# Kernel tuning notes

Hardware: AMD Instinct MI355X
Metric: run time of the kernel (lower is better)

The kernel has to match this reference:

```python
import jax, jax.numpy as jnp
import numpy as np

D_MODEL = 1024
N_HEADS = 16
D_HEAD = D_MODEL // N_HEADS
D_FF = 4 * D_MODEL
SEQ = 2048
BATCH = 4
EPS = 1e-5


def setup_inputs() -> dict:
    key = jax.random.key(0)
    ks = jax.random.split(key, 12)
    s = 0.02
    return {
        "x": jax.random.normal(ks[0], (BATCH, SEQ, D_MODEL), dtype=jnp.float32),
        "ln1_g": jnp.ones((D_MODEL,), jnp.float32),
        "ln1_b": jnp.zeros((D_MODEL,), jnp.float32),
        "wq": jax.random.normal(ks[1], (N_HEADS, D_MODEL, D_HEAD), jnp.float32) * s,
        "bq": jnp.zeros((N_HEADS, D_HEAD), jnp.float32),
        "wk": jax.random.normal(ks[2], (N_HEADS, D_MODEL, D_HEAD), jnp.float32) * s,
        "bk": jnp.zeros((N_HEADS, D_HEAD), jnp.float32),
        "wv": jax.random.normal(ks[3], (N_HEADS, D_MODEL, D_HEAD), jnp.float32) * s,
        "bv": jnp.zeros((N_HEADS, D_HEAD), jnp.float32),
        "wp": jax.random.normal(ks[4], (D_MODEL, D_MODEL), jnp.float32) * s,
        "bp": jnp.zeros((D_MODEL,), jnp.float32),
        "ln2_g": jnp.ones((D_MODEL,), jnp.float32),
        "ln2_b": jnp.zeros((D_MODEL,), jnp.float32),
        "w1": jax.random.normal(ks[5], (D_MODEL, D_FF), jnp.float32) * s,
        "b1": jnp.zeros((D_FF,), jnp.float32),
        "w2": jax.random.normal(ks[6], (D_FF, D_MODEL), jnp.float32) * s,
        "b2": jnp.zeros((D_MODEL,), jnp.float32),
    }


def _layer_norm(x, g, b):
    mu = jnp.mean(x, axis=-1, keepdims=True)
    var = jnp.mean(jnp.square(x - mu), axis=-1, keepdims=True)
    return (x - mu) * jax.lax.rsqrt(var + EPS) * g + b


def _block(x, ln1_g, ln1_b, wq, bq, wk, bk, wv, bv, wp, bp,
           ln2_g, ln2_b, w1, b1, w2, b2):
    B, S, D = x.shape
    # --- pre-LN multi-head causal self-attention ---
    xn = _layer_norm(x, ln1_g, ln1_b)
    q = jnp.einsum('bsd,hde->bhse', xn, wq) + bq[None, :, None, :]
    k = jnp.einsum('bsd,hde->bhse', xn, wk) + bk[None, :, None, :]
    v = jnp.einsum('bsd,hde->bhse', xn, wv) + bv[None, :, None, :]
    scores = jnp.einsum('bhse,bhte->bhst', q, k) / np.sqrt(D_HEAD).astype(np.float32)
    causal = jnp.tril(jnp.ones((S, S), dtype=bool))
    scores = jnp.where(causal[None, None], scores, jnp.float32(-jnp.inf))
    attn = jax.nn.softmax(scores, axis=-1)
    o = jnp.einsum('bhst,bhte->bhse', attn, v)          # [B,H,S,Dh]
    o = o.transpose(0, 2, 1, 3).reshape(B, S, D)         # concat heads
    x = x + o @ wp + bp
    # --- pre-LN feedforward ---
    xn2 = _layer_norm(x, ln2_g, ln2_b)
    h = jax.nn.relu(xn2 @ w1 + b1)
    x = x + h @ w2 + b2
    return x


def reference(x, ln1_g, ln1_b, wq, bq, wk, bk, wv, bv, wp, bp,
              ln2_g, ln2_b, w1, b1, w2, b2):
    return _block(x, ln1_g, ln1_b, wq, bq, wk, bk, wv, bv, wp, bp,
                  ln2_g, ln2_b, w1, b1, w2, b2)
```

## Files before the change

### kernel.cpp

```cpp
#include <hip/hip_runtime.h>
#include <hip/hip_bf16.h>

#define D_MODEL 1024
#define N_HEADS 16
#define D_HEAD  64
#define D_FF    4096
#define SEQ     2048
#define BATCH   4
#define NROWS   (BATCH * SEQ)

typedef __attribute__((ext_vector_type(8))) short short8;
typedef __attribute__((ext_vector_type(4))) float f32x4;

#define EXP2(x) exp2f(x)
#define MFMA16(a, b, c) __builtin_amdgcn_mfma_f32_16x16x32_bf16(a, b, c, 0, 0, 0)

static __device__ __forceinline__ ushort f2bf(float x) {
  __hip_bfloat16 h = __float2bfloat16(x);
  return *reinterpret_cast<ushort*>(&h);
}
static __device__ __forceinline__ float bf2f(ushort u) {
  unsigned int v = ((unsigned int)u) << 16;
  return *reinterpret_cast<float*>(&v);
}

static __device__ __forceinline__ void gl_lds16(const ushort* g, ushort* l) {
  __builtin_amdgcn_global_load_lds(
      (const __attribute__((address_space(1))) void*)g,
      (__attribute__((address_space(3))) void*)l, 16, 0, 0);
}

struct PackArgs {
  const float* in[6];
  ushort* out[6];
  int K[6], N[6], nx[6], per_batch[6];
  long in_bs[6], out_bs[6];
  int cum[7];
};

__global__ __launch_bounds__(256) void pack_all(PackArgs a) {
  const int b = blockIdx.x;
  int j = 0;
#pragma unroll
  for (int i = 0; i < 5; ++i) if (b >= a.cum[i + 1]) j = i + 1;
  const int tidx = b - a.cum[j];
  const int bz = tidx / a.per_batch[j];
  const int rem = tidx % a.per_batch[j];
  const int n0 = (rem % a.nx[j]) * 32;
  const int k0 = (rem / a.nx[j]) * 32;
  const float* in = a.in[j] + (long)bz * a.in_bs[j];
  ushort* out = a.out[j] + (long)bz * a.out_bs[j];
  const int K = a.K[j], N = a.N[j];

  __shared__ float tile[32][33];
  const int tx = threadIdx.x, ty = threadIdx.y;
#pragma unroll
  for (int i = 0; i < 32; i += 8)
    tile[ty + i][tx] = in[(size_t)(k0 + ty + i) * N + n0 + tx];
  __syncthreads();
#pragma unroll
  for (int i = 0; i < 32; i += 8)
    out[(size_t)(n0 + ty + i) * K + k0 + tx] = f2bf(tile[tx][ty + i]);
}

__global__ __launch_bounds__(256) void ln_kernel(
    const float* __restrict__ x, const float* __restrict__ g,
    const float* __restrict__ b, ushort* __restrict__ out) {
  int row = blockIdx.x, t = threadIdx.x;
  const float4 v = *(const float4*)(x + (size_t)row * D_MODEL + t * 4);
  float s  = v.x + v.y + v.z + v.w;
  float ss = v.x * v.x + v.y * v.y + v.z * v.z + v.w * v.w;
#pragma unroll
  for (int off = 1; off < 64; off <<= 1) {
    s  += __shfl_xor(s, off, 64);
    ss += __shfl_xor(ss, off, 64);
  }
  __shared__ float rs_[4], rss_[4];
  int w = t >> 6;
  if ((t & 63) == 0) { rs_[w] = s; rss_[w] = ss; }
  __syncthreads();
  s  = rs_[0] + rs_[1] + rs_[2] + rs_[3];
  ss = rss_[0] + rss_[1] + rss_[2] + rss_[3];
  float mu  = s * (1.0f / D_MODEL);
  float var = ss * (1.0f / D_MODEL) - mu * mu;
  float rstd = rsqrtf(var + 1e-5f);
  float4 gg = *(const float4*)(g + t * 4);
  float4 bb = *(const float4*)(b + t * 4);
  ushort4 r;
  r.x = f2bf((v.x - mu) * rstd * gg.x + bb.x);
  r.y = f2bf((v.y - mu) * rstd * gg.y + bb.y);
  r.z = f2bf((v.z - mu) * rstd * gg.z + bb.z);
  r.w = f2bf((v.w - mu) * rstd * gg.w + bb.w);
  *(ushort4*)(out + (size_t)row * D_MODEL + t * 4) = r;
}

__global__ __launch_bounds__(256) void ln_bf16_kernel(
    const ushort* __restrict__ x, const float* __restrict__ g,
    const float* __restrict__ b, ushort* __restrict__ out) {
  int row = blockIdx.x, t = threadIdx.x;
  const ushort4 u = *(const ushort4*)(x + (size_t)row * D_MODEL + t * 4);
  float4 v;
  v.x = bf2f(u.x); v.y = bf2f(u.y); v.z = bf2f(u.z); v.w = bf2f(u.w);
  float s  = v.x + v.y + v.z + v.w;
  float ss = v.x * v.x + v.y * v.y + v.z * v.z + v.w * v.w;
#pragma unroll
  for (int off = 1; off < 64; off <<= 1) {
    s  += __shfl_xor(s, off, 64);
    ss += __shfl_xor(ss, off, 64);
  }
  __shared__ float rs_[4], rss_[4];
  int w = t >> 6;
  if ((t & 63) == 0) { rs_[w] = s; rss_[w] = ss; }
  __syncthreads();
  s  = rs_[0] + rs_[1] + rs_[2] + rs_[3];
  ss = rss_[0] + rss_[1] + rss_[2] + rss_[3];
  float mu  = s * (1.0f / D_MODEL);
  float var = ss * (1.0f / D_MODEL) - mu * mu;
  float rstd = rsqrtf(var + 1e-5f);
  float4 gg = *(const float4*)(g + t * 4);
  float4 bb = *(const float4*)(b + t * 4);
  ushort4 r;
  r.x = f2bf((v.x - mu) * rstd * gg.x + bb.x);
  r.y = f2bf((v.y - mu) * rstd * gg.y + bb.y);
  r.z = f2bf((v.z - mu) * rstd * gg.z + bb.z);
  r.w = f2bf((v.w - mu) * rstd * gg.w + bb.w);
  *(ushort4*)(out + (size_t)row * D_MODEL + t * 4) = r;
}

template <int MODE>
__global__ __launch_bounds__(512, 2) void gemm256(
    const ushort* __restrict__ A, const ushort* __restrict__ BT,
    int M, int N, int K,
    const float* __restrict__ bias0, const float* __restrict__ bias1,
    const float* __restrict__ bias2,
    void* __restrict__ out0, void* __restrict__ out1, void* __restrict__ out2) {
  __shared__ __align__(16) ushort As[2][256 * 64];
  __shared__ __align__(16) ushort Bs[2][256 * 64];
  const int gx = N >> 8;
  const int nwg = gx * (M >> 8);
  const int cpx = nwg >> 3;
  const int tile = (blockIdx.x & 7) * cpx + (blockIdx.x >> 3);
  const int bn = tile % gx, bm = tile / gx;
  const int t = threadIdx.x, lane = t & 63, w = t >> 6;
  const int wr = w >> 2, wc = w & 3;
  const int l16 = lane & 15, l4 = lane >> 4;

  const ushort* Ab = A + (size_t)(bm * 256) * K;
  const ushort* Bb = BT + (size_t)(bn * 256) * K;

  int srow[4], scol[4];
#pragma unroll
  for (int i = 0; i < 4; ++i) {
    int c = i * 512 + t;
    srow[i] = c >> 3;
    scol[i] = 8 * ((c & 7) ^ ((c >> 3) & 7));
  }

  f32x4 acc[8][4] = {};
  int cur = 0;
  const int nk = K >> 6;

#pragma unroll
  for (int i = 0; i < 4; ++i) {
    gl_lds16(&Ab[(size_t)srow[i] * K + scol[i]], (ushort*)&As[0][(i * 512 + w * 64) * 8]);
    gl_lds16(&Bb[(size_t)srow[i] * K + scol[i]], (ushort*)&Bs[0][(i * 512 + w * 64) * 8]);
  }

  for (int kt = 0; kt < nk; ++kt) {
    if (kt + 1 < nk) {
      const int k0n = (kt + 1) << 6;
#pragma unroll
      for (int i = 0; i < 4; ++i) {
        gl_lds16(&Ab[(size_t)srow[i] * K + k0n + scol[i]], (ushort*)&As[cur ^ 1][(i * 512 + w * 64) * 8]);
        gl_lds16(&Bb[(size_t)srow[i] * K + k0n + scol[i]], (ushort*)&Bs[cur ^ 1][(i * 512 + w * 64) * 8]);
      }
      asm volatile("s_waitcnt vmcnt(8)" ::: "memory");
    } else {
      asm volatile("s_waitcnt vmcnt(0)" ::: "memory");
    }
    __builtin_amdgcn_s_barrier();

    const ushort* As_ = As[cur];
    const ushort* Bs_ = Bs[cur];
    short8 bfr[4][2];
#pragma unroll
    for (int n = 0; n < 4; ++n) {
      const int row = wc * 64 + n * 16 + l16;
      const int sw = (row & 7) * 8;
      bfr[n][0] = *(const short8*)&Bs_[row * 64 + ((l4 * 8) ^ sw)];
      bfr[n][1] = *(const short8*)&Bs_[row * 64 + ((l4 * 8 + 32) ^ sw)];
    }
#pragma unroll
    for (int m = 0; m < 8; ++m) {
      const int row = wr * 128 + m * 16 + l16;
      const int sw = (row & 7) * 8;
      short8 a0 = *(const short8*)&As_[row * 64 + ((l4 * 8) ^ sw)];
      short8 a1 = *(const short8*)&As_[row * 64 + ((l4 * 8 + 32) ^ sw)];
#pragma unroll
      for (int n = 0; n < 4; ++n) {
        acc[m][n] = MFMA16(a0, bfr[n][0], acc[m][n]);
        acc[m][n] = MFMA16(a1, bfr[n][1], acc[m][n]);
      }
    }
    asm volatile("" ::: "memory");
    __builtin_amdgcn_s_barrier();
    cur ^= 1;
  }

  const int row0 = bm * 256 + wr * 128, col0 = bn * 256 + wc * 64;
#pragma unroll
  for (int m = 0; m < 8; ++m) {
#pragma unroll
    for (int n = 0; n < 4; ++n) {
      const int col = col0 + n * 16 + l16;
      if (MODE == 0) {
        const int which = col >> 10;
        const int c = col & 1023;
        if (which < 2) {
          const float* bp_ = (which == 0) ? bias0 : bias1;
          ushort* op = (which == 0) ? (ushort*)out0 : (ushort*)out1;
          const float scale = (which == 0) ? 0.125f * 1.44269504f : 1.0f;
#pragma unroll
          for (int i = 0; i < 4; ++i) {
            const int row = row0 + m * 16 + l4 * 4 + i;
            op[(size_t)row * D_MODEL + c] = f2bf((acc[m][n][i] + bp_[c]) * scale);
          }
        } else {
          const int d = c & 63, hh2 = c >> 6;
          const float bv_ = bias2[c];
          ushort4 r4;
          r4.x = f2bf(acc[m][n][0] + bv_);
          r4.y = f2bf(acc[m][n][1] + bv_);
          r4.z = f2bf(acc[m][n][2] + bv_);
          r4.w = f2bf(acc[m][n][3] + bv_);
          const int row = row0 + m * 16 + l4 * 4;
          const int bb2 = row >> 11, s = row & 2047;
          *(ushort4*)((ushort*)out2 + ((size_t)(bb2 * 16 + hh2) * 64 + d) * SEQ + s) = r4;
        }
      } else {
#pragma unroll
        for (int i = 0; i < 4; ++i) {
          const int row = row0 + m * 16 + l4 * 4 + i;
          const float val = fmaxf(acc[m][n][i] + bias0[col], 0.0f);
          ((ushort*)out0)[(size_t)row * D_FF + col] = f2bf(val);
        }
      }
    }
  }
}

template <int RMODE>
__global__ __launch_bounds__(256, 2) void gemm128d(
    const ushort* __restrict__ A, const ushort* __restrict__ BT,
    int M, int N, int K,
    const float* __restrict__ bias0, const void* __restrict__ resid,
    void* __restrict__ out0) {
  __shared__ __align__(16) ushort As[2][128 * 64];
  __shared__ __align__(16) ushort Bs[2][128 * 64];
  const int gx = N >> 7;
  const int nwg = gx * (M >> 7);
  const int cpx = nwg >> 3;
  const int tile = (blockIdx.x & 7) * cpx + (blockIdx.x >> 3);
  const int bn = tile % gx, bm = tile / gx;
  const int t = threadIdx.x, lane = t & 63, w = t >> 6;
  const int wr = w >> 1, wc = w & 1;
  const int l16 = lane & 15, l4 = lane >> 4;

  const ushort* Ab = A + (size_t)(bm * 128) * K;
  const ushort* Bb = BT + (size_t)(bn * 128) * K;

  int srow[4], scol[4];
#pragma unroll
  for (int i = 0; i < 4; ++i) {
    int c = i * 256 + t;
    srow[i] = c >> 3;
    scol[i] = 8 * ((c & 7) ^ ((c >> 3) & 7));
  }

  f32x4 acc[4][4] = {};
  int cur = 0;
  const int nk = K >> 6;

#pragma unroll
  for (int i = 0; i < 4; ++i) {
    gl_lds16(&Ab[(size_t)srow[i] * K + scol[i]], (ushort*)&As[0][(i * 256 + w * 64) * 8]);
    gl_lds16(&Bb[(size_t)srow[i] * K + scol[i]], (ushort*)&Bs[0][(i * 256 + w * 64) * 8]);
  }

  for (int kt = 0; kt < nk; ++kt) {
    if (kt + 1 < nk) {
      const int k0n = (kt + 1) << 6;
#pragma unroll
      for (int i = 0; i < 4; ++i) {
        gl_lds16(&Ab[(size_t)srow[i] * K + k0n + scol[i]], (ushort*)&As[cur ^ 1][(i * 256 + w * 64) * 8]);
        gl_lds16(&Bb[(size_t)srow[i] * K + k0n + scol[i]], (ushort*)&Bs[cur ^ 1][(i * 256 + w * 64) * 8]);
      }
      asm volatile("s_waitcnt vmcnt(8)" ::: "memory");
    } else {
      asm volatile("s_waitcnt vmcnt(0)" ::: "memory");
    }
    __builtin_amdgcn_s_barrier();

    const ushort* As_ = As[cur];
    const ushort* Bs_ = Bs[cur];
    short8 bfr[4][2];
#pragma unroll
    for (int n = 0; n < 4; ++n) {
      const int row = wc * 64 + n * 16 + l16;
      const int sw = (row & 7) * 8;
      bfr[n][0] = *(const short8*)&Bs_[row * 64 + ((l4 * 8) ^ sw)];
      bfr[n][1] = *(const short8*)&Bs_[row * 64 + ((l4 * 8 + 32) ^ sw)];
    }
    __builtin_amdgcn_s_setprio(1);
#pragma unroll
    for (int m = 0; m < 4; ++m) {
      const int row = wr * 64 + m * 16 + l16;
      const int sw = (row & 7) * 8;
      short8 a0 = *(const short8*)&As_[row * 64 + ((l4 * 8) ^ sw)];
      short8 a1 = *(const short8*)&As_[row * 64 + ((l4 * 8 + 32) ^ sw)];
#pragma unroll
      for (int n = 0; n < 4; ++n) {
        acc[m][n] = MFMA16(a0, bfr[n][0], acc[m][n]);
        acc[m][n] = MFMA16(a1, bfr[n][1], acc[m][n]);
      }
    }
    __builtin_amdgcn_s_setprio(0);
    asm volatile("" ::: "memory");
    __builtin_amdgcn_s_barrier();
    cur ^= 1;
  }

  const int row0 = bm * 128 + wr * 64, col0 = bn * 128 + wc * 64;
#pragma unroll
  for (int m = 0; m < 4; ++m) {
#pragma unroll
    for (int n = 0; n < 4; ++n) {
      const int col = col0 + n * 16 + l16;
#pragma unroll
      for (int i = 0; i < 4; ++i) {
        const int row = row0 + m * 16 + l4 * 4 + i;
        const size_t idx = (size_t)row * D_MODEL + col;
        if (RMODE == 0) {
          const float rv = ((const float*)resid)[idx];
          ((ushort*)out0)[idx] = f2bf(acc[m][n][i] + bias0[col] + rv);
        } else {
          const float rv = bf2f(((const ushort*)resid)[idx]);
          ((float*)out0)[idx] = acc[m][n][i] + bias0[col] + rv;
        }
      }
    }
  }
}

__global__ __launch_bounds__(256) void attn8_kernel(
    const ushort* __restrict__ Q, const ushort* __restrict__ Km,
    const ushort* __restrict__ Vt, ushort* __restrict__ O) {
  const int b = blockIdx.x;
  const int bh = (b & 7) * 8 + ((b >> 3) & 7);
  const int p = b >> 6;
  const int bb = bh >> 4, hh = bh & 15;
  const int t = threadIdx.x, lane = t & 63, w = t >> 6;
  const int l16 = lane & 15, l4 = lane >> 4;
  const size_t base  = (size_t)bb * SEQ * D_MODEL + (size_t)hh * 64;
  const size_t vbase = (size_t)bh * 64 * SEQ;

  __shared__ __align__(16) ushort Ks[4][64 * 64];
  __shared__ __align__(16) ushort Vs[4][64 * 64];
  __shared__ __align__(16) ushort Pw[4][32 * 64];
  ushort* myP = &Pw[w][0];

#define STAGE(ktile, buf) do {                                                     \
    const int kv0_ = (ktile) * 64;                                                 \
    _Pragma("unroll")                                                              \
    for (int i_ = 0; i_ < 2; ++i_) {                                               \
      const int g_ = i_ * 256 + t;                                                 \
      const int row_ = g_ >> 3;                                                    \
      const int c8_ = ((g_ & 7) ^ (row_ & 7)) * 8;                                 \
      gl_lds16(&Km[base + (size_t)(kv0_ + row_) * D_MODEL + c8_],                  \
               (ushort*)&Ks[buf][(i_ * 256 + w * 64) * 8]);                        \
      gl_lds16(&Vt[vbase + (size_t)row_ * SEQ + kv0_ + c8_],                       \
               (ushort*)&Vs[buf][(i_ * 256 + w * 64) * 8]);                        \
    }                                                                              \
  } while (0)

#pragma unroll
  for (int pan = 0; pan < 2; ++pan) {
    const int qt = pan ? p : (15 - p);
    const int qb = qt * 128 + w * 32;
    const int nt = qt * 2 + 2;

    short8 qf[2][2];
#pragma unroll
    for (int qj = 0; qj < 2; ++qj)
#pragma unroll
      for (int dk = 0; dk < 2; ++dk)
        qf[qj][dk] = *(const short8*)&Q[base + (size_t)(qb + qj * 16 + l16) * D_MODEL + dk * 32 + l4 * 8];

    f32x4 oacc[4][2] = {};
    float l_i[2] = {0.0f, 0.0f};

    STAGE(0, 0);
    STAGE(1, 1);

    for (int jt = 0; jt < nt; jt += 2) {
      if (jt + 2 < nt) {
        STAGE(jt + 2, (jt + 2) & 3);
        STAGE(jt + 3, (jt + 3) & 3);
        asm volatile("s_waitcnt vmcnt(8)" ::: "memory");
      } else {
        asm volatile("s_waitcnt vmcnt(0)" ::: "memory");
      }
      __builtin_amdgcn_s_barrier();

#pragma unroll
      for (int half = 0; half < 2; ++half) {
        const int kt = jt + half;
        const int kv0 = kt * 64;
        const bool active = (kv0 <= qb + 31);
        if (active) {
          const ushort* Kc = Ks[kt & 3];
          const ushort* Vc = Vs[kt & 3];

          f32x4 sacc[2][4] = {};
#pragma unroll
          for (int n = 0; n < 4; ++n) {
            const int r = n * 16 + l16;
            const int rs = r * 8, rx = r & 7;
#pragma unroll
            for (int dk = 0; dk < 2; ++dk) {
              short8 ak = *(const short8*)&Kc[(rs + ((dk * 4 + l4) ^ rx)) * 8];
              sacc[0][n] = MFMA16(ak, qf[0][dk], sacc[0][n]);
              sacc[1][n] = MFMA16(ak, qf[1][dk], sacc[1][n]);
            }
          }

          const bool diag = (kv0 + 63 > qb);
#pragma unroll
          for (int qj = 0; qj < 2; ++qj) {
            const int qq = qb + qj * 16 + l16;
            const int ql = qj * 16 + l16;
            const int psw = (ql & 7) * 8;
            if (diag) {
#pragma unroll
              for (int n = 0; n < 4; ++n)
#pragma unroll
                for (int i = 0; i < 4; ++i) {
                  const int kv = kv0 + n * 16 + l4 * 4 + i;
                  if (kv > qq) sacc[qj][n][i] = -1e30f;
                }
            }
            float lsum = 0.0f;
#pragma unroll
            for (int n = 0; n < 4; ++n) {
              const float p0 = EXP2(sacc[qj][n][0]);
              const float p1 = EXP2(sacc[qj][n][1]);
              const float p2 = EXP2(sacc[qj][n][2]);
              const float p3 = EXP2(sacc[qj][n][3]);
              lsum += p0 + p1 + p2 + p3;
              ushort4 pk;
              pk.x = f2bf(p0); pk.y = f2bf(p1); pk.z = f2bf(p2); pk.w = f2bf(p3);
              *(ushort4*)&myP[ql * 64 + ((n * 16 + l4 * 4) ^ psw)] = pk;
            }
            l_i[qj] += lsum;
          }

#pragma unroll
          for (int kk = 0; kk < 2; ++kk) {
            short8 bp[2];
#pragma unroll
            for (int qj = 0; qj < 2; ++qj) {
              const int ql = qj * 16 + l16;
              bp[qj] = *(const short8*)&myP[ql * 64 + ((kk * 32 + l4 * 8) ^ ((ql & 7) * 8))];
            }
#pragma unroll
            for (int nd = 0; nd < 4; ++nd) {
              const int r = nd * 16 + l16;
              short8 av = *(const short8*)&Vc[(r * 8 + ((kk * 4 + l4) ^ (r & 7))) * 8];
              oacc[nd][0] = MFMA16(av, bp[0], oacc[nd][0]);
              oacc[nd][1] = MFMA16(av, bp[1], oacc[nd][1]);
            }
          }
        }
      }

      asm volatile("" ::: "memory");
      __builtin_amdgcn_s_barrier();
    }

#pragma unroll
    for (int qj = 0; qj < 2; ++qj) {
      l_i[qj] += __shfl_xor(l_i[qj], 16, 64);
      l_i[qj] += __shfl_xor(l_i[qj], 32, 64);
      const int qq = qb + qj * 16 + l16;
      const float inv = 1.0f / l_i[qj];
#pragma unroll
      for (int nd = 0; nd < 4; ++nd) {
        ushort4 r;
        r.x = f2bf(oacc[nd][qj][0] * inv);
        r.y = f2bf(oacc[nd][qj][1] * inv);
        r.z = f2bf(oacc[nd][qj][2] * inv);
        r.w = f2bf(oacc[nd][qj][3] * inv);
        *(ushort4*)&O[base + (size_t)qq * D_MODEL + nd * 16 + l4 * 4] = r;
      }
    }
  }
#undef STAGE
}

extern "C" void kernel_launch(void* const* d_in, const int* in_sizes, int n_in,
                              void* d_out, int out_size, void* d_ws, size_t ws_size,
                              hipStream_t stream) {
  const float* x    = (const float*)d_in[0];
  const float* ln1g = (const float*)d_in[1];
  const float* ln1b = (const float*)d_in[2];
  const float* wq   = (const float*)d_in[3];
  const float* bq   = (const float*)d_in[4];
  const float* wk   = (const float*)d_in[5];
  const float* bk   = (const float*)d_in[6];
  const float* wv   = (const float*)d_in[7];
  const float* bv   = (const float*)d_in[8];
  const float* wp   = (const float*)d_in[9];
  const float* bp   = (const float*)d_in[10];
  const float* ln2g = (const float*)d_in[11];
  const float* ln2b = (const float*)d_in[12];
  const float* w1   = (const float*)d_in[13];
  const float* b1   = (const float*)d_in[14];
  const float* w2   = (const float*)d_in[15];
  const float* b2   = (const float*)d_in[16];
  float* out = (float*)d_out;

  char* base = (char*)d_ws;
  size_t off = 0;
  auto alloc = [&](size_t bytes) -> void* {
    void* r = base + off;
    off += (bytes + 255) & ~(size_t)255;
    return r;
  };
  ushort* WqkvT = (ushort*)alloc((size_t)3 * D_MODEL * D_MODEL * 2);
  ushort* WpT   = (ushort*)alloc((size_t)D_MODEL * D_MODEL * 2);
  ushort* W1T   = (ushort*)alloc((size_t)D_FF * D_MODEL * 2);
  ushort* W2T   = (ushort*)alloc((size_t)D_MODEL * D_FF * 2);
  ushort* xn    = (ushort*)alloc((size_t)NROWS * D_MODEL * 2);
  ushort* q     = (ushort*)alloc((size_t)NROWS * D_MODEL * 2);
  ushort* k     = (ushort*)alloc((size_t)NROWS * D_MODEL * 2);
  ushort* vt    = (ushort*)alloc((size_t)NROWS * D_MODEL * 2);
  ushort* o     = (ushort*)alloc((size_t)NROWS * D_MODEL * 2);
  ushort* x2    = (ushort*)alloc((size_t)NROWS * D_MODEL * 2);
  ushort* xn2   = (ushort*)alloc((size_t)NROWS * D_MODEL * 2);
  ushort* hbuf  = (ushort*)alloc((size_t)NROWS * D_FF * 2);

  PackArgs pa;
  pa.in[0] = wq; pa.out[0] = WqkvT + (size_t)0 * D_MODEL * D_MODEL;
  pa.in[1] = wk; pa.out[1] = WqkvT + (size_t)1 * D_MODEL * D_MODEL;
  pa.in[2] = wv; pa.out[2] = WqkvT + (size_t)2 * D_MODEL * D_MODEL;
  pa.in[3] = wp; pa.out[3] = WpT;
  pa.in[4] = w1; pa.out[4] = W1T;
  pa.in[5] = w2; pa.out[5] = W2T;
  for (int j = 0; j < 3; ++j) {
    pa.K[j] = D_MODEL; pa.N[j] = D_HEAD; pa.nx[j] = 2; pa.per_batch[j] = 64;
    pa.in_bs[j] = (long)D_MODEL * D_HEAD; pa.out_bs[j] = (long)D_HEAD * D_MODEL;
  }
  pa.K[3] = D_MODEL; pa.N[3] = D_MODEL; pa.nx[3] = 32; pa.per_batch[3] = 1024;
  pa.in_bs[3] = 0; pa.out_bs[3] = 0;
  pa.K[4] = D_MODEL; pa.N[4] = D_FF; pa.nx[4] = 128; pa.per_batch[4] = 4096;
  pa.in_bs[4] = 0; pa.out_bs[4] = 0;
  pa.K[5] = D_FF; pa.N[5] = D_MODEL; pa.nx[5] = 32; pa.per_batch[5] = 4096;
  pa.in_bs[5] = 0; pa.out_bs[5] = 0;
  pa.cum[0] = 0; pa.cum[1] = 1024; pa.cum[2] = 2048; pa.cum[3] = 3072;
  pa.cum[4] = 4096; pa.cum[5] = 8192; pa.cum[6] = 12288;
  pack_all<<<12288, dim3(32, 8), 0, stream>>>(pa);

  ln_kernel<<<NROWS, 256, 0, stream>>>(x, ln1g, ln1b, xn);
  gemm256<0><<<dim3((NROWS / 256) * (3 * D_MODEL / 256)), 512, 0, stream>>>(
      xn, WqkvT, NROWS, 3 * D_MODEL, D_MODEL, bq, bk, bv, q, k, vt);
  attn8_kernel<<<512, 256, 0, stream>>>(q, k, vt, o);
  gemm128d<0><<<dim3((NROWS / 128) * (D_MODEL / 128)), 256, 0, stream>>>(
      o, WpT, NROWS, D_MODEL, D_MODEL, bp, x, x2);
  ln_bf16_kernel<<<NROWS, 256, 0, stream>>>(x2, ln2g, ln2b, xn2);
  gemm256<2><<<dim3((NROWS / 256) * (D_FF / 256)), 512, 0, stream>>>(
      xn2, W1T, NROWS, D_FF, D_MODEL, b1, nullptr, nullptr, hbuf, nullptr, nullptr);
  gemm128d<1><<<dim3((NROWS / 128) * (D_MODEL / 128)), 256, 0, stream>>>(
      hbuf, W2T, NROWS, D_MODEL, D_FF, b2, x2, out);
}
```

Measured before the change: 346.6 us.

## Fuse first layernorm into weight-pack launch and raise MFMA wave priority

Result: no change. 351.3 us (+1.4%).

```diff
diff --git a/kernel.cpp b/kernel.cpp
--- a/kernel.cpp
+++ b/kernel.cpp
@@ -36,10 +36,44 @@
   int K[6], N[6], nx[6], per_batch[6];
   long in_bs[6], out_bs[6];
   int cum[7];
+  const float* lnx; const float* lng; const float* lnb; ushort* lnout;
 };
 
-__global__ __launch_bounds__(256) void pack_all(PackArgs a) {
+__global__ __launch_bounds__(256) void pack_ln(PackArgs a) {
   const int b = blockIdx.x;
+  __shared__ float tile[32][33];
+
+  if (b >= a.cum[6]) {
+    const int row = b - a.cum[6];
+    const int t = threadIdx.y * 32 + threadIdx.x;
+    const float4 v = *(const float4*)(a.lnx + (size_t)row * D_MODEL + t * 4);
+    float s  = v.x + v.y + v.z + v.w;
+    float ss = v.x * v.x + v.y * v.y + v.z * v.z + v.w * v.w;
+#pragma unroll
+    for (int off = 1; off < 64; off <<= 1) {
+      s  += __shfl_xor(s, off, 64);
+      ss += __shfl_xor(ss, off, 64);
+    }
+    float* red = &tile[0][0];
+    const int w = t >> 6;
+    if ((t & 63) == 0) { red[w] = s; red[4 + w] = ss; }
+    __syncthreads();
+    s  = red[0] + red[1] + red[2] + red[3];
+    ss = red[4] + red[5] + red[6] + red[7];
+    const float mu  = s * (1.0f / D_MODEL);
+    const float var = ss * (1.0f / D_MODEL) - mu * mu;
+    const float rstd = rsqrtf(var + 1e-5f);
+    const float4 gg = *(const float4*)(a.lng + t * 4);
+    const float4 bb = *(const float4*)(a.lnb + t * 4);
+    ushort4 r;
+    r.x = f2bf((v.x - mu) * rstd * gg.x + bb.x);
+    r.y = f2bf((v.y - mu) * rstd * gg.y + bb.y);
+    r.z = f2bf((v.z - mu) * rstd * gg.z + bb.z);
+    r.w = f2bf((v.w - mu) * rstd * gg.w + bb.w);
+    *(ushort4*)(a.lnout + (size_t)row * D_MODEL + t * 4) = r;
+    return;
+  }
+
   int j = 0;
 #pragma unroll
   for (int i = 0; i < 5; ++i) if (b >= a.cum[i + 1]) j = i + 1;
@@ -52,7 +86,6 @@
   ushort* out = a.out[j] + (long)bz * a.out_bs[j];
   const int K = a.K[j], N = a.N[j];
 
-  __shared__ float tile[32][33];
   const int tx = threadIdx.x, ty = threadIdx.y;
 #pragma unroll
   for (int i = 0; i < 32; i += 8)
@@ -63,11 +96,13 @@
     out[(size_t)(n0 + ty + i) * K + k0 + tx] = f2bf(tile[tx][ty + i]);
 }
 
-__global__ __launch_bounds__(256) void ln_kernel(
-    const float* __restrict__ x, const float* __restrict__ g,
+__global__ __launch_bounds__(256) void ln_bf16_kernel(
+    const ushort* __restrict__ x, const float* __restrict__ g,
     const float* __restrict__ b, ushort* __restrict__ out) {
   int row = blockIdx.x, t = threadIdx.x;
-  const float4 v = *(const float4*)(x + (size_t)row * D_MODEL + t * 4);
+  const ushort4 u = *(const ushort4*)(x + (size_t)row * D_MODEL + t * 4);
+  float4 v;
+  v.x = bf2f(u.x); v.y = bf2f(u.y); v.z = bf2f(u.z); v.w = bf2f(u.w);
   float s  = v.x + v.y + v.z + v.w;
   float ss = v.x * v.x + v.y * v.y + v.z * v.z + v.w * v.w;
 #pragma unroll
@@ -94,39 +129,6 @@
   *(ushort4*)(out + (size_t)row * D_MODEL + t * 4) = r;
 }
 
-__global__ __launch_bounds__(256) void ln_bf16_kernel(
-    const ushort* __restrict__ x, const float* __restrict__ g,
-    const float* __restrict__ b, ushort* __restrict__ out) {
-  int row = blockIdx.x, t = threadIdx.x;
-  const ushort4 u = *(const ushort4*)(x + (size_t)row * D_MODEL + t * 4);
-  float4 v;
-  v.x = bf2f(u.x); v.y = bf2f(u.y); v.z = bf2f(u.z); v.w = bf2f(u.w);
-  float s  = v.x + v.y + v.z + v.w;
-  float ss = v.x * v.x + v.y * v.y + v.z * v.z + v.w * v.w;
-#pragma unroll
-  for (int off = 1; off < 64; off <<= 1) {
-    s  += __shfl_xor(s, off, 64);
-    ss += __shfl_xor(ss, off, 64);
-  }
-  __shared__ float rs_[4], rss_[4];
-  int w = t >> 6;
-  if ((t & 63) == 0) { rs_[w] = s; rss_[w] = ss; }
-  __syncthreads();
-  s  = rs_[0] + rs_[1] + rs_[2] + rs_[3];
-  ss = rss_[0] + rss_[1] + rss_[2] + rss_[3];
-  float mu  = s * (1.0f / D_MODEL);
-  float var = ss * (1.0f / D_MODEL) - mu * mu;
-  float rstd = rsqrtf(var + 1e-5f);
-  float4 gg = *(const float4*)(g + t * 4);
-  float4 bb = *(const float4*)(b + t * 4);
-  ushort4 r;
-  r.x = f2bf((v.x - mu) * rstd * gg.x + bb.x);
-  r.y = f2bf((v.y - mu) * rstd * gg.y + bb.y);
-  r.z = f2bf((v.z - mu) * rstd * gg.z + bb.z);
-  r.w = f2bf((v.w - mu) * rstd * gg.w + bb.w);
-  *(ushort4*)(out + (size_t)row * D_MODEL + t * 4) = r;
-}
-
 template <int MODE>
 __global__ __launch_bounds__(512, 2) void gemm256(
     const ushort* __restrict__ A, const ushort* __restrict__ BT,
@@ -190,6 +192,7 @@
       bfr[n][0] = *(const short8*)&Bs_[row * 64 + ((l4 * 8) ^ sw)];
       bfr[n][1] = *(const short8*)&Bs_[row * 64 + ((l4 * 8 + 32) ^ sw)];
     }
+    __builtin_amdgcn_s_setprio(1);
 #pragma unroll
     for (int m = 0; m < 8; ++m) {
       const int row = wr * 128 + m * 16 + l16;
@@ -202,6 +205,7 @@
         acc[m][n] = MFMA16(a1, bfr[n][1], acc[m][n]);
       }
     }
+    __builtin_amdgcn_s_setprio(0);
     asm volatile("" ::: "memory");
     __builtin_amdgcn_s_barrier();
     cur ^= 1;
@@ -422,6 +426,7 @@
           const ushort* Vc = Vs[kt & 3];
 
           f32x4 sacc[2][4] = {};
+          __builtin_amdgcn_s_setprio(1);
 #pragma unroll
           for (int n = 0; n < 4; ++n) {
             const int r = n * 16 + l16;
@@ -433,6 +438,7 @@
               sacc[1][n] = MFMA16(ak, qf[1][dk], sacc[1][n]);
             }
           }
+          __builtin_amdgcn_s_setprio(0);
 
           const bool diag = (kv0 + 63 > qb);
 #pragma unroll
@@ -464,6 +470,7 @@
             l_i[qj] += lsum;
           }
 
+          __builtin_amdgcn_s_setprio(1);
 #pragma unroll
           for (int kk = 0; kk < 2; ++kk) {
             short8 bp[2];
@@ -480,6 +487,7 @@
               oacc[nd][1] = MFMA16(av, bp[1], oacc[nd][1]);
             }
           }
+          __builtin_amdgcn_s_setprio(0);
         }
       }
 
@@ -568,9 +576,9 @@
   pa.in_bs[5] = 0; pa.out_bs[5] = 0;
   pa.cum[0] = 0; pa.cum[1] = 1024; pa.cum[2] = 2048; pa.cum[3] = 3072;
   pa.cum[4] = 4096; pa.cum[5] = 8192; pa.cum[6] = 12288;
-  pack_all<<<12288, dim3(32, 8), 0, stream>>>(pa);
-
-  ln_kernel<<<NROWS, 256, 0, stream>>>(x, ln1g, ln1b, xn);
+  pa.lnx = x; pa.lng = ln1g; pa.lnb = ln1b; pa.lnout = xn;
+  pack_ln<<<12288 + NROWS, dim3(32, 8), 0, stream>>>(pa);
+
   gemm256<0><<<dim3((NROWS / 256) * (3 * D_MODEL / 256)), 512, 0, stream>>>(
       xn, WqkvT, NROWS, 3 * D_MODEL, D_MODEL, bq, bk, bv, q, k, vt);
   attn8_kernel<<<512, 256, 0, stream>>>(q, k, vt, o);
```
